# Kernel tuning notes

Hardware: AMD Instinct MI355X
Metric: run time of the kernel (lower is better)

The kernel has to match this reference:

```python
import jax, jax.numpy as jnp
import numpy as np
import math

V, D, H, DFF, NL, CTX = 32000, 512, 8, 2048, 2, 1024
B, S = 2, 1024

def ln(x, w, eps=1e-5):
    mu = jnp.mean(x, axis=-1, keepdims=True)
    var = jnp.var(x, axis=-1, keepdims=True)
    return (x - mu) / jnp.sqrt(var + eps) * w

def setup_inputs() -> dict:
    key = jax.random.key(0)
    ks = jax.random.split(key, 10)
    inp = {
        "x": jax.random.randint(ks[0], (B, S), 0, V),
        "wte": jax.random.normal(ks[1], (V, D), jnp.float32) * 0.02,
        "wpe": jax.random.normal(ks[2], (CTX + 1, D), jnp.float32) * 0.02,
        "ln_e_w": jnp.ones((D,), jnp.float32),
        "ln_p_w": jnp.ones((D,), jnp.float32),
        "ln_f_w": jnp.ones((D,), jnp.float32),
        "ln_mlp_w": jnp.ones((D,), jnp.float32),
        "W_q_diag": jax.random.normal(ks[3], (H, D), jnp.float32) * 0.02,
        "W_k_diag": jax.random.normal(ks[4], (H, D), jnp.float32) * 0.02,
        "W_o": jax.random.normal(ks[5], (NL, D, D * H), jnp.float32) * (0.02 / math.sqrt(2 * NL)),
        "mlp_w1": jax.random.normal(ks[6], (DFF, D), jnp.float32) * 0.02,
        "mlp_w2": jax.random.normal(ks[7], (D, DFF), jnp.float32) * 0.02,
    }
    return inp

def reference(x, wte, wpe, ln_e_w, ln_p_w, ln_f_w, ln_mlp_w, W_q_diag, W_k_diag, W_o, mlp_w1, mlp_w2):
    Bsz, Sl = x.shape
    e = ln(wte[x], ln_e_w)                       # (B,S,D)
    p = ln(wpe[: Sl + 1], ln_p_w)                # (S+1,D), identical across batch
    Q = p[1:][None, :, :] * W_q_diag[:, None, :]   # (H,S,D)
    K = p[:-1][None, :, :] * W_k_diag[:, None, :]  # (H,S,D)
    krn = jnp.einsum('hsd,htd->hst', Q, K) / math.sqrt(D)
    mask = jnp.tril(jnp.ones((Sl, Sl), bool))
    krn = jnp.where(mask[None], krn, 0.0)        # (H,S,S)
    wn = 1.0 / (jnp.arange(Sl, dtype=jnp.float32) + 1.0)  # W_N diagonal

    f_k = jnp.zeros_like(e)
    for i in range(NL):
        # R = softmax over S of (V,D)@(B,D,S) -> (B,V,S)
        R = jax.nn.softmax(jnp.einsum('vd,bsd->bvs', wte, f_k), axis=-1)
        ex_wte = jnp.einsum('bvs,vd->bsd', R, wte)
        ex_wte = ex_wte / jnp.sum(R, axis=1)[..., None]  # normalize by sum over V
        Vt = e - ex_wte                                   # (B,S,D)
        delta = jnp.einsum('hst,btd->bhsd', krn, Vt)      # (B,H,S,D)
        delta = delta * wn[None, None, :, None]           # W_N row scaling
        delta = jnp.transpose(delta, (0, 2, 1, 3)).reshape(Bsz, Sl, H * D)
        delta = delta @ W_o[i].T                          # (B,S,D)
        f_k = f_k + delta
        # use_ff MLP block
        h = ln(f_k, ln_mlp_w)
        f_k = f_k + jax.nn.gelu(h @ mlp_w1.T, approximate=False) @ mlp_w2.T

    out = ln(f_k, ln_f_w)
    logits = out[:, -1:, :] @ wte.T               # (B,1,V), targets=None branch
    return logits
```

## Files before the change

### kernel.cpp

```cpp
#include <hip/hip_runtime.h>

#define DV   512
#define SV   1024
#define BV   2
#define VV   32000
#define HV   8
#define DFFV 2048
#define NLV  2
#define KCX  25

typedef __bf16 bf16;
typedef __bf16 bf16x4 __attribute__((ext_vector_type(4)));
typedef __bf16 bf16x8 __attribute__((ext_vector_type(8)));
typedef float  f32x4  __attribute__((ext_vector_type(4)));

__device__ __forceinline__ void lds_dma16(const void* g, void* l) {
  __builtin_amdgcn_global_load_lds(
      (const __attribute__((address_space(1))) unsigned int*)g,
      (__attribute__((address_space(3))) unsigned int*)l,
      16, 0, 0);
}

template<typename OUT>
__device__ __forceinline__ void row_ln_512(const float* __restrict__ src,
                                           const float* __restrict__ w,
                                           OUT* __restrict__ dst, int lane) {
  const float4 a = *(const float4*)(src + lane*8);
  const float4 b = *(const float4*)(src + lane*8 + 4);
  float s = a.x+a.y+a.z+a.w + b.x+b.y+b.z+b.w;
  float q = a.x*a.x+a.y*a.y+a.z*a.z+a.w*a.w + b.x*b.x+b.y*b.y+b.z*b.z+b.w*b.w;
#pragma unroll
  for (int off = 32; off > 0; off >>= 1) {
    s += __shfl_down(s, off, 64);
    q += __shfl_down(q, off, 64);
  }
  s = __shfl(s, 0, 64); q = __shfl(q, 0, 64);
  const float mu   = s * (1.0f/512.0f);
  const float rstd = rsqrtf(q * (1.0f/512.0f) - mu*mu + 1e-5f);
  const float4 wa = *(const float4*)(w + lane*8);
  const float4 wb = *(const float4*)(w + lane*8 + 4);
  OUT* d = dst + lane*8;
  d[0] = (OUT)((a.x-mu)*rstd*wa.x);
  d[1] = (OUT)((a.y-mu)*rstd*wa.y);
  d[2] = (OUT)((a.z-mu)*rstd*wa.z);
  d[3] = (OUT)((a.w-mu)*rstd*wa.w);
  d[4] = (OUT)((b.x-mu)*rstd*wb.x);
  d[5] = (OUT)((b.y-mu)*rstd*wb.y);
  d[6] = (OUT)((b.z-mu)*rstd*wb.z);
  d[7] = (OUT)((b.w-mu)*rstd*wb.w);
}

__global__ void embed_ln_k(const int* __restrict__ x, const float* __restrict__ wte,
                           const float* __restrict__ w, float* __restrict__ e, int nrows) {
  int row = blockIdx.x * 4 + (threadIdx.x >> 6);
  if (row >= nrows) return;
  int tok = x[row];
  row_ln_512<float>(wte + (long)tok * DV, w, e + (long)row * DV, threadIdx.x & 63);
}

__global__ void rows_ln_f32_k(const float* __restrict__ src, const float* __restrict__ w,
                              float* __restrict__ dst, int nrows) {
  int row = blockIdx.x * 4 + (threadIdx.x >> 6);
  if (row >= nrows) return;
  row_ln_512<float>(src + (long)row * DV, w, dst + (long)row * DV, threadIdx.x & 63);
}

__global__ void rows_ln_bf16_k(const float* __restrict__ src, const float* __restrict__ w,
                               bf16* __restrict__ dst, int nrows) {
  int row = blockIdx.x * 4 + (threadIdx.x >> 6);
  if (row >= nrows) return;
  row_ln_512<bf16>(src + (long)row * DV, w, dst + (long)row * DV, threadIdx.x & 63);
}

__global__ void final_ln_k(const float* __restrict__ f_k, const float* __restrict__ w,
                           float* __restrict__ obuf) {
  int b = threadIdx.x >> 6;
  if (b >= BV) return;
  row_ln_512<float>(f_k + ((long)b * SV + (SV - 1)) * DV, w, obuf + (long)b * DV,
                    threadIdx.x & 63);
}

__global__ void cast_f2b_k(const float* __restrict__ in, bf16* __restrict__ o, long n) {
  long i = ((long)blockIdx.x * 256 + threadIdx.x) * 4;
  if (i >= n) return;
  float4 v = *(const float4*)(in + i);
  o[i+0] = (bf16)v.x; o[i+1] = (bf16)v.y; o[i+2] = (bf16)v.z; o[i+3] = (bf16)v.w;
}

__global__ void wte_prep_k(const float* __restrict__ wte, bf16* __restrict__ wb,
                           bf16* __restrict__ wbT, float* __restrict__ wm) {
  __shared__ float t[32][33];
  __shared__ float cpart[8][32];
  const int d0 = blockIdx.x * 32, v0 = blockIdx.y * 32;
  const int tx = threadIdx.x, ty = threadIdx.y;
  float csum = 0.f;
#pragma unroll
  for (int k = 0; k < 4; k++) {
    const int vl = ty*4 + k;
    const float val = wte[(long)(v0+vl)*DV + d0+tx];
    t[vl][tx] = val;
    csum += val;
  }
  cpart[ty][tx] = csum;
  __syncthreads();
  const int tid = ty*32 + tx;
  const int r = tid >> 3, c = (tid & 7) * 4;
  {
    bf16x4 o;
    o[0] = (bf16)t[r][c];   o[1] = (bf16)t[r][c+1];
    o[2] = (bf16)t[r][c+2]; o[3] = (bf16)t[r][c+3];
    *(bf16x4*)(&wb[(long)(v0+r)*DV + d0+c]) = o;
  }
  {
    bf16x4 o;
    o[0] = (bf16)t[c][r];   o[1] = (bf16)t[c+1][r];
    o[2] = (bf16)t[c+2][r]; o[3] = (bf16)t[c+3][r];
    *(bf16x4*)(&wbT[(long)(d0+r)*VV + v0+c]) = o;
  }
  if (ty == 0) {
    float s = 0.f;
#pragma unroll
    for (int k = 0; k < 8; k++) s += cpart[k][tx];
    atomicAdd(&wm[d0+tx], s);
  }
}

__global__ void qk_prep_k(const float* __restrict__ pn, const float* __restrict__ Wq,
                          const float* __restrict__ Wk, bf16* __restrict__ Qh,
                          bf16* __restrict__ Kh) {
  const int s = blockIdx.x, hh = blockIdx.y;
  const int d = threadIdx.x * 4;
  const float4 q  = *(const float4*)(pn + (long)(s+1)*DV + d);
  const float4 kk = *(const float4*)(pn + (long)s*DV + d);
  const float4 aq = *(const float4*)(Wq + (long)hh*DV + d);
  const float4 ak = *(const float4*)(Wk + (long)hh*DV + d);
  const long o = ((long)hh*SV + s)*DV + d;
  Qh[o+0]=(bf16)(q.x*aq.x);  Qh[o+1]=(bf16)(q.y*aq.y);
  Qh[o+2]=(bf16)(q.z*aq.z);  Qh[o+3]=(bf16)(q.w*aq.w);
  Kh[o+0]=(bf16)(kk.x*ak.x); Kh[o+1]=(bf16)(kk.y*ak.y);
  Kh[o+2]=(bf16)(kk.z*ak.z); Kh[o+3]=(bf16)(kk.w*ak.w);
}

__global__ void colsum_reduce_k(const float* __restrict__ part, float* __restrict__ cs) {
  const int s = blockIdx.x * 256 + threadIdx.x;
  float acc = 0.f;
  for (int v = 0; v < VV/128; v++) acc += part[(long)v * SV + s];
  cs[s] = acc;
}

__global__ void freduce_k(const float* __restrict__ part, float* __restrict__ f_k, int KC) {
  const long i = ((long)blockIdx.x * 256 + threadIdx.x) * 4;
  const int  b = (int)(i / ((long)SV*DV));
  const long r = i % ((long)SV*DV);
  float4 acc = *(const float4*)(f_k + i);
  for (int c = 0; c < KC; c++) {
    const float4 v = *(const float4*)(part + ((long)(b*KC + c))*SV*DV + r);
    acc.x += v.x; acc.y += v.y; acc.z += v.z; acc.w += v.w;
  }
  *(float4*)(f_k + i) = acc;
}

__global__ void vt_part_k(const float* __restrict__ e, const bf16* __restrict__ pb,
                          const float* __restrict__ cs, bf16* __restrict__ VtT) {
  __shared__ float t[32][33];
  const int d0 = blockIdx.x * 32, s0 = blockIdx.y * 32;
  const int tx = threadIdx.x, ty = threadIdx.y;
#pragma unroll
  for (int k = 0; k < 4; k++) {
    const int sl = ty + k*8;
    const long off = (long)(s0+sl)*DV + d0+tx;
    float acc = 0.f;
    for (int c = 0; c < KCX; c++) acc += (float)pb[(long)c*SV*DV + off];
    t[sl][tx] = e[off] - acc / cs[s0 + sl];
  }
  __syncthreads();
#pragma unroll
  for (int k = 0; k < 4; k++) {
    const int dl = ty + k*8;
    VtT[(long)(d0+dl)*SV + s0+tx] = (bf16)t[tx][dl];
  }
}

__global__ void vt0_transpose_k(const float* __restrict__ e, const float* __restrict__ wm,
                                bf16* __restrict__ VtT) {
  __shared__ float t[32][33];
  const int d0 = blockIdx.x * 32, s0 = blockIdx.y * 32;
  const int tx = threadIdx.x, ty = threadIdx.y;
  const float mval = wm[d0 + tx] * (1.0f / (float)VV);
#pragma unroll
  for (int k = 0; k < 4; k++) {
    const int sl = ty + k*8;
    t[sl][tx] = e[(long)(s0+sl)*DV + d0+tx] - mval;
  }
  __syncthreads();
#pragma unroll
  for (int k = 0; k < 4; k++) {
    const int dl = ty + k*8;
    VtT[(long)(d0+dl)*SV + s0+tx] = (bf16)t[tx][dl];
  }
}

__global__ void logits_k(const float* __restrict__ obuf, const float* __restrict__ wte,
                         float* __restrict__ out, int V) {
  const int wv = threadIdx.x >> 6, lane = threadIdx.x & 63;
  const int v = blockIdx.x * 4 + wv;
  const float* wr = wte + (long)v * DV;
  const float4 a  = *(const float4*)(wr + lane*8);
  const float4 c  = *(const float4*)(wr + lane*8 + 4);
  const float4 oa0 = *(const float4*)(obuf + lane*8);
  const float4 ob0 = *(const float4*)(obuf + lane*8 + 4);
  const float4 oa1 = *(const float4*)(obuf + DV + lane*8);
  const float4 ob1 = *(const float4*)(obuf + DV + lane*8 + 4);
  float d0 = a.x*oa0.x + a.y*oa0.y + a.z*oa0.z + a.w*oa0.w
           + c.x*ob0.x + c.y*ob0.y + c.z*ob0.z + c.w*ob0.w;
  float d1 = a.x*oa1.x + a.y*oa1.y + a.z*oa1.z + a.w*oa1.w
           + c.x*ob1.x + c.y*ob1.y + c.z*ob1.z + c.w*ob1.w;
#pragma unroll
  for (int off = 32; off > 0; off >>= 1) {
    d0 += __shfl_down(d0, off, 64);
    d1 += __shfl_down(d1, off, 64);
  }
  if (lane == 0) { out[v] = d0; out[(long)V + v] = d1; }
}

__device__ __forceinline__ long xcd_swz(long lin, long nwg) {
  const long qq = nwg >> 3, rr = nwg & 7;
  const long xcd = lin & 7, idx = lin >> 3;
  return (xcd < rr ? xcd * (qq + 1) : rr * (qq + 1) + (xcd - rr) * qq) + idx;
}

struct GemmArgs {
  const bf16* A; const bf16* B;
  float* Cf; bf16* Cb;
  int K, lda, ldb, ldc;
  long sAh, sAb, sBh, sBb, sCh, sCb;
  int Hmod, KC, causal, swap;
  float scale;
};

template<int EPI>
__global__ __launch_bounds__(256)
void gemm_nt(GemmArgs g) {
  __shared__ bf16 As[2][128*32];
  __shared__ bf16 Bs[2][128*32];
  const int tid = threadIdx.x;
  int bx = blockIdx.x, by = blockIdx.y, z = blockIdx.z;
  {
    const int nbx = gridDim.x, nby = gridDim.y;
    const long nwg = (long)nbx * nby * gridDim.z;
    long lin = xcd_swz(bx + (long)nbx * (by + (long)nby * z), nwg);
    bx = (int)(lin % nbx);
    const long t2 = lin / nbx;
    by = (int)(t2 % nby);
    z  = (int)(t2 / nby);
  }
  const int chunk = z % g.KC;
  const int zo = z / g.KC;
  const int h = zo % g.Hmod;
  const int b = zo / g.Hmod;
  if (g.swap) { int t = bx; bx = by; by = t; }
  const int m0 = by * 128;
  const int n0 = bx * 128;
  const long coff = (long)h * g.sCh + (long)b * g.sCb;

  if (EPI == 3 && n0 > m0 + 127) return;

  const bf16* A = g.A + (long)h * g.sAh + (long)b * g.sAb;
  const bf16* B = g.B + (long)h * g.sBh + (long)b * g.sBb;
  const int lane = tid & 63;
  const int wv = tid >> 6;
  const int wm = (wv >> 1) * 64;
  const int wn = (wv & 1) * 64;
  const int frow = lane & 15;
  const int quad = lane >> 4;
  const int sg8  = ((lane & 3) ^ ((lane >> 3) & 3)) * 8;
  const int drow = lane >> 2;

  const f32x4 fzero = {0.f, 0.f, 0.f, 0.f};
  f32x4 acc[4][4];
#pragma unroll
  for (int i = 0; i < 4; i++)
#pragma unroll
    for (int j = 0; j < 4; j++) acc[i][j] = fzero;

  int k0, klen;
  if (g.causal) { k0 = 0; klen = min(g.K, m0 + 128); }
  else          { klen = g.K / g.KC; k0 = chunk * klen; }

  auto stage = [&](int buf, int kk) {
#pragma unroll
    for (int c = 0; c < 2; c++) {
      const int rb = c*64 + wv*16;
      lds_dma16(A + (long)(m0 + rb + drow) * g.lda + kk + sg8, &As[buf][rb*32]);
      lds_dma16(B + (long)(n0 + rb + drow) * g.ldb + kk + sg8, &Bs[buf][rb*32]);
    }
  };

  const int nsteps = klen >> 5;
  int cur = 0;
  stage(0, k0);
  for (int it = 0; it < nsteps; ++it) {
    if (it + 1 < nsteps) {
      stage(cur ^ 1, k0 + (it + 1) * 32);
      asm volatile("s_waitcnt vmcnt(4)" ::: "memory");
    } else {
      asm volatile("s_waitcnt vmcnt(0)" ::: "memory");
    }
    __builtin_amdgcn_s_barrier();
    bf16x8 af[4], bfr[4];
    const int sw = (frow >> 1) & 3;
#pragma unroll
    for (int i = 0; i < 4; i++)
      af[i] = *(const bf16x8*)(&As[cur][(wm + i*16 + frow)*32 + ((quad ^ sw))*8]);
#pragma unroll
    for (int j = 0; j < 4; j++)
      bfr[j] = *(const bf16x8*)(&Bs[cur][(wn + j*16 + frow)*32 + ((quad ^ sw))*8]);
#pragma unroll
    for (int i = 0; i < 4; i++)
#pragma unroll
      for (int j = 0; j < 4; j++)
        acc[i][j] = __builtin_amdgcn_mfma_f32_16x16x32_bf16(af[i], bfr[j], acc[i][j], 0, 0, 0);
    __builtin_amdgcn_s_barrier();
    cur ^= 1;
  }

  const int rb = quad * 4;
#pragma unroll
  for (int i = 0; i < 4; i++) {
#pragma unroll
    for (int j = 0; j < 4; j++) {
#pragma unroll
      for (int r = 0; r < 4; r++) {
        const int gm = m0 + wm + i*16 + rb + r;
        const int gn = n0 + wn + j*16 + frow;
        const float v = acc[i][j][r];
        if (EPI == 2) {
          g.Cb[coff + (long)gm * g.ldc + gn] = (bf16)v;
        } else if (EPI == 3) {
          const float val = (gn <= gm) ? v * g.scale / (float)(gm + 1) : 0.0f;
          g.Cb[coff + (long)gm * g.ldc + gn] = (bf16)val;
        } else if (EPI == 4) {
          const float ge = 0.5f * v * (1.0f + erff(v * 0.70710678118f));
          g.Cb[coff + (long)gm * g.ldc + gn] = (bf16)ge;
        } else if (EPI == 6) {
          g.Cf[(long)(b*g.KC + chunk) * g.sCh + (long)gm * g.ldc + gn] = v;
        } else if (EPI == 7) {
          g.Cb[(long)chunk * g.sCh + (long)gm * g.ldc + gn] = (bf16)v;
        }
      }
    }
  }
}

template<int EPI>
__global__ __launch_bounds__(512)
void gemm256(GemmArgs g) {
  __shared__ bf16 As[2][256*64];
  __shared__ bf16 Bs[2][256*64];
  const int tid = threadIdx.x;
  int bm = blockIdx.x, bn = blockIdx.y, z = blockIdx.z;
  {
    const int nbx = gridDim.x, nby = gridDim.y;
    const long nwg = (long)nbx * nby * gridDim.z;
    long lin = xcd_swz(bm + (long)nbx * (bn + (long)nby * z), nwg);
    bm = (int)(lin % nbx);
    const long t2 = lin / nbx;
    bn = (int)(t2 % nby);
    z  = (int)(t2 / nby);
  }
  const int m0 = bm * 256, n0 = bn * 256;
  const int lane = tid & 63, wv = tid >> 6;
  const int wm = (wv >> 2) * 128, wn = (wv & 3) * 64;
  const int frow = lane & 15, quad = lane >> 4;
  const int sg8  = ((lane & 7) ^ (lane >> 3)) * 8;
  const int drow = lane >> 3;

  const f32x4 fzero = {0.f, 0.f, 0.f, 0.f};
  f32x4 acc[8][4];
#pragma unroll
  for (int i = 0; i < 8; i++)
#pragma unroll
    for (int j = 0; j < 4; j++) acc[i][j] = fzero;

  const int klen = g.K / g.KC;
  const int k0 = z * klen;

  auto stage = [&](int buf, int kk) {
#pragma unroll
    for (int c = 0; c < 4; c++) {
      const int rb = c*64 + wv*8;
      lds_dma16(g.A + (long)(m0 + rb + drow) * g.lda + kk + sg8, &As[buf][rb*64]);
      lds_dma16(g.B + (long)(n0 + rb + drow) * g.ldb + kk + sg8, &Bs[buf][rb*64]);
    }
  };

  const int nsteps = klen >> 6;
  int cur = 0;
  stage(0, k0);
  for (int it = 0; it < nsteps; ++it) {
    if (it + 1 < nsteps) {
      stage(cur ^ 1, k0 + (it + 1) * 64);
      asm volatile("s_waitcnt vmcnt(8)" ::: "memory");
    } else {
      asm volatile("s_waitcnt vmcnt(0)" ::: "memory");
    }
    __builtin_amdgcn_s_barrier();
    const int sw = frow & 7;
#pragma unroll
    for (int ks = 0; ks < 2; ks++) {
      bf16x8 af[8], bfr[4];
#pragma unroll
      for (int j = 0; j < 4; j++)
        bfr[j] = *(const bf16x8*)(&Bs[cur][(wn + j*16 + frow)*64 + (((ks*4 + quad) ^ sw))*8]);
#pragma unroll
      for (int i = 0; i < 8; i++)
        af[i] = *(const bf16x8*)(&As[cur][(wm + i*16 + frow)*64 + (((ks*4 + quad) ^ sw))*8]);
#pragma unroll
      for (int i = 0; i < 8; i++)
#pragma unroll
        for (int j = 0; j < 4; j++)
          acc[i][j] = __builtin_amdgcn_mfma_f32_16x16x32_bf16(af[i], bfr[j], acc[i][j], 0, 0, 0);
    }
    __builtin_amdgcn_s_barrier();
    cur ^= 1;
  }

  const int rb4 = quad * 4;
  if (EPI == 5) {
    const int vblk = (n0 + wn) >> 7;
#pragma unroll
    for (int i = 0; i < 8; i++) {
#pragma unroll
      for (int r = 0; r < 4; r++) {
        const int gm = m0 + wm + i*16 + rb4 + r;
        float rs = 0.f;
#pragma unroll
        for (int j = 0; j < 4; j++) {
          const int gn = n0 + wn + j*16 + frow;
          const float ev = __expf(acc[i][j][r]);
          g.Cb[(long)gm * g.ldc + gn] = (bf16)ev;
          rs += ev;
        }
#pragma unroll
        for (int off = 1; off < 16; off <<= 1)
          rs += __shfl_xor(rs, off, 64);
        if (frow == 0) atomicAdd(g.Cf + (long)vblk * SV + gm, rs);
      }
    }
  } else {
#pragma unroll
    for (int i = 0; i < 8; i++) {
#pragma unroll
      for (int j = 0; j < 4; j++) {
#pragma unroll
        for (int r = 0; r < 4; r++) {
          const int gm = m0 + wm + i*16 + rb4 + r;
          const int gn = n0 + wn + j*16 + frow;
          g.Cb[(long)z * g.sCh + (long)gm * g.ldc + gn] = (bf16)acc[i][j][r];
        }
      }
    }
  }
}

static void layer_tail(int il, bf16* krn, bf16* VtT, bf16* U_rs, bf16* Wo_b,
                       float* f_k, bf16* f_k_b, bf16* hbuf, bf16* Gbuf, float* fpart,
                       bf16* w1_b, bf16* w2_b, const float* lnmw, int do_cast,
                       hipStream_t stream) {
  {
    GemmArgs g = {};
    g.A = krn; g.B = VtT; g.Cb = U_rs;
    g.K = SV; g.lda = SV; g.ldb = SV; g.ldc = HV*DV;
    g.sAh = (long)SV*SV; g.sBb = (long)DV*SV;
    g.sCh = DV; g.sCb = (long)SV*HV*DV;
    g.Hmod = HV; g.KC = 1; g.causal = 1;
    gemm_nt<2><<<dim3(DV/128, SV/128, BV*HV), 256, 0, stream>>>(g);
  }
  {
    GemmArgs g = {};
    g.A = U_rs; g.B = Wo_b + (long)il*DV*HV*DV; g.Cf = fpart;
    g.K = HV*DV; g.lda = HV*DV; g.ldb = HV*DV; g.ldc = DV;
    g.sAb = (long)SV*HV*DV; g.sCh = (long)SV*DV;
    g.Hmod = 1; g.KC = 8; g.causal = 0;
    gemm_nt<6><<<dim3(DV/128, SV/128, BV*8), 256, 0, stream>>>(g);
  }
  freduce_k<<<dim3(BV*SV*DV/4/256), 256, 0, stream>>>(fpart, f_k, 8);
  rows_ln_bf16_k<<<dim3(BV*SV/4), 256, 0, stream>>>(f_k, lnmw, hbuf, BV*SV);
  {
    GemmArgs g = {};
    g.A = hbuf; g.B = w1_b; g.Cb = Gbuf;
    g.K = DV; g.lda = DV; g.ldb = DV; g.ldc = DFFV;
    g.sAb = (long)SV*DV; g.sCb = (long)SV*DFFV;
    g.Hmod = 1; g.KC = 1; g.causal = 0;
    gemm_nt<4><<<dim3(DFFV/128, SV/128, BV), 256, 0, stream>>>(g);
  }
  {
    GemmArgs g = {};
    g.A = Gbuf; g.B = w2_b; g.Cf = fpart;
    g.K = DFFV; g.lda = DFFV; g.ldb = DFFV; g.ldc = DV;
    g.sAb = (long)SV*DFFV; g.sCh = (long)SV*DV;
    g.Hmod = 1; g.KC = 8; g.causal = 0;
    gemm_nt<6><<<dim3(DV/128, SV/128, BV*8), 256, 0, stream>>>(g);
  }
  freduce_k<<<dim3(BV*SV*DV/4/256), 256, 0, stream>>>(fpart, f_k, 8);
  if (do_cast)
    cast_f2b_k<<<dim3((BV*SV*DV/4+255)/256), 256, 0, stream>>>(f_k, f_k_b, (long)BV*SV*DV);
}

extern "C" void kernel_launch(void* const* d_in, const int* in_sizes, int n_in,
                              void* d_out, int out_size, void* d_ws, size_t ws_size,
                              hipStream_t stream) {
  const int*   x    = (const int*)d_in[0];
  const float* wte  = (const float*)d_in[1];
  const float* wpe  = (const float*)d_in[2];
  const float* lnew = (const float*)d_in[3];
  const float* lnpw = (const float*)d_in[4];
  const float* lnfw = (const float*)d_in[5];
  const float* lnmw = (const float*)d_in[6];
  const float* Wq   = (const float*)d_in[7];
  const float* Wk   = (const float*)d_in[8];
  const float* Wo   = (const float*)d_in[9];
  const float* w1   = (const float*)d_in[10];
  const float* w2   = (const float*)d_in[11];
  float* out = (float*)d_out;
  (void)in_sizes; (void)n_in; (void)out_size; (void)ws_size;

  char* p = (char*)d_ws;
  auto alloc = [&](size_t bytes) -> void* {
    void* r = (void*)p;
    p += (bytes + 255) & ~(size_t)255;
    return r;
  };
  float* e      = (float*)alloc((size_t)BV*SV*DV*4);
  float* pn     = (float*)alloc((size_t)(SV+1)*DV*4);
  bf16*  wteT_b = (bf16*)alloc((size_t)DV*VV*2);
  bf16*  wte_b  = (bf16*)alloc((size_t)VV*DV*2);
  bf16*  krn    = (bf16*)alloc((size_t)HV*SV*SV*2);
  bf16*  Wo_b   = (bf16*)alloc((size_t)NLV*DV*HV*DV*2);
  bf16*  w1_b   = (bf16*)alloc((size_t)DFFV*DV*2);
  bf16*  w2_b   = (bf16*)alloc((size_t)DV*DFFV*2);
  float* f_k    = (float*)alloc((size_t)BV*SV*DV*4);
  bf16*  f_k_b  = (bf16*)alloc((size_t)BV*SV*DV*2);
  bf16*  expart = (bf16*)alloc((size_t)KCX*SV*DV*2);
  bf16*  VtT    = (bf16*)alloc((size_t)BV*DV*SV*2);
  bf16*  hbuf   = (bf16*)alloc((size_t)BV*SV*DV*2);
  float* colsum = (float*)alloc((size_t)SV*4);
  float* part   = (float*)alloc((size_t)(VV/128)*SV*4);
  float* obuf   = (float*)alloc((size_t)BV*DV*4);
  float* wmean  = (float*)alloc((size_t)DV*4);
  char*  arena  = (char*)alloc((size_t)SV*VV*2);
  bf16*  Qh     = (bf16*)arena;
  bf16*  Kh     = (bf16*)(arena + (size_t)HV*SV*DV*2);
  bf16*  PT     = (bf16*)arena;
  bf16*  U_rs   = (bf16*)arena;
  bf16*  Gbuf   = (bf16*)(arena + (size_t)BV*SV*HV*DV*2);
  float* fpart  = (float*)(arena + (size_t)BV*SV*HV*DV*2 + (size_t)BV*SV*DFFV*2);

  hipMemsetAsync(f_k,   0, (size_t)BV*SV*DV*4, stream);
  hipMemsetAsync(f_k_b, 0, (size_t)BV*SV*DV*2, stream);
  hipMemsetAsync(wmean, 0, (size_t)DV*4, stream);
  wte_prep_k<<<dim3(DV/32, VV/32), dim3(32,8), 0, stream>>>(wte, wte_b, wteT_b, wmean);
  cast_f2b_k<<<dim3((NLV*DV*HV*DV/4+255)/256), 256, 0, stream>>>(Wo, Wo_b, (long)NLV*DV*HV*DV);
  cast_f2b_k<<<dim3((DFFV*DV/4+255)/256), 256, 0, stream>>>(w1, w1_b, (long)DFFV*DV);
  cast_f2b_k<<<dim3((DV*DFFV/4+255)/256), 256, 0, stream>>>(w2, w2_b, (long)DV*DFFV);
  embed_ln_k<<<dim3(BV*SV/4), 256, 0, stream>>>(x, wte, lnew, e, BV*SV);
  rows_ln_f32_k<<<dim3((SV+1+3)/4), 256, 0, stream>>>(wpe, lnpw, pn, SV+1);
  qk_prep_k<<<dim3(SV, HV), 128, 0, stream>>>(pn, Wq, Wk, Qh, Kh);

  {
    GemmArgs g = {};
    g.A = Qh; g.B = Kh; g.Cb = krn;
    g.K = DV; g.lda = DV; g.ldb = DV; g.ldc = SV;
    g.sAh = (long)SV*DV; g.sBh = (long)SV*DV; g.sCh = (long)SV*SV;
    g.Hmod = HV; g.KC = 1; g.causal = 0;
    g.scale = 0.044194173824159216f;
    gemm_nt<3><<<dim3(SV/128, SV/128, HV), 256, 0, stream>>>(g);
  }

  for (int b = 0; b < BV; b++)
    vt0_transpose_k<<<dim3(DV/32, SV/32), dim3(32,8), 0, stream>>>(
        e + (long)b*SV*DV, wmean, VtT + (long)b*DV*SV);
  layer_tail(0, krn, VtT, U_rs, Wo_b, f_k, f_k_b, hbuf, Gbuf, fpart,
             w1_b, w2_b, lnmw, 1, stream);

  for (int b = 0; b < BV; b++) {
    hipMemsetAsync(part, 0, (size_t)(VV/128)*SV*4, stream);
    {
      GemmArgs g = {};
      g.A = f_k_b + (long)b*SV*DV; g.B = wte_b; g.Cb = PT; g.Cf = part;
      g.K = DV; g.lda = DV; g.ldb = DV; g.ldc = VV;
      g.KC = 1;
      gemm256<5><<<dim3(SV/256, VV/256, 1), 512, 0, stream>>>(g);
    }
    colsum_reduce_k<<<dim3(SV/256), 256, 0, stream>>>(part, colsum);
    {
      GemmArgs g = {};
      g.A = PT; g.B = wteT_b; g.Cb = expart;
      g.K = VV; g.lda = VV; g.ldb = VV; g.ldc = DV;
      g.sCh = (long)SV*DV;
      g.KC = KCX;
      gemm256<7><<<dim3(SV/256, DV/256, KCX), 512, 0, stream>>>(g);
    }
    vt_part_k<<<dim3(DV/32, SV/32), dim3(32,8), 0, stream>>>(
        e + (long)b*SV*DV, expart, colsum, VtT + (long)b*DV*SV);
  }
  layer_tail(1, krn, VtT, U_rs, Wo_b, f_k, f_k_b, hbuf, Gbuf, fpart,
             w1_b, w2_b, lnmw, 0, stream);

  final_ln_k<<<1, 256, 0, stream>>>(f_k, lnfw, obuf);
  logits_k<<<dim3(VV/4), 256, 0, stream>>>(obuf, wte, out, VV);
}
```

Baseline: 537.9 us.

## Restructure gemm256 main loop into 8-wave ping-pong with split-K LDS halves

Reorganizes the 256x256 GEMM kernel's LDS tiles into two 32-wide K halves per buffer and rewrites the main loop into four phases. Each phase interleaves finer-grained global->LDS DMA stages with LDS fragment loads and an MFMA cluster, using s_setprio and sched_barrier to separate memory and compute phases across waves. The swizzle pattern changes to fit the 32-element row layout. This aims to hide load latency and reduce register pressure by holding only four A fragments at a time, at the cost of more barriers per iteration and more fragile vmcnt bookkeeping.

```diff
diff --git a/kernel.cpp b/kernel.cpp
--- a/kernel.cpp
+++ b/kernel.cpp
@@ -355,8 +355,8 @@
 template<int EPI>
 __global__ __launch_bounds__(512)
 void gemm256(GemmArgs g) {
-  __shared__ bf16 As[2][256*64];
-  __shared__ bf16 Bs[2][256*64];
+  __shared__ bf16 As[2][2][256*32];
+  __shared__ bf16 Bs[2][2][256*32];
   const int tid = threadIdx.x;
   int bm = blockIdx.x, bn = blockIdx.y, z = blockIdx.z;
   {
@@ -372,8 +372,7 @@
   const int lane = tid & 63, wv = tid >> 6;
   const int wm = (wv >> 2) * 128, wn = (wv & 3) * 64;
   const int frow = lane & 15, quad = lane >> 4;
-  const int sg8  = ((lane & 7) ^ (lane >> 3)) * 8;
-  const int drow = lane >> 3;
+  const int sg8 = ((lane & 3) ^ ((lane >> 3) & 3)) * 8;
 
   const f32x4 fzero = {0.f, 0.f, 0.f, 0.f};
   f32x4 acc[8][4];
@@ -385,44 +384,103 @@
   const int klen = g.K / g.KC;
   const int k0 = z * klen;
 
-  auto stage = [&](int buf, int kk) {
-#pragma unroll
-    for (int c = 0; c < 4; c++) {
-      const int rb = c*64 + wv*8;
-      lds_dma16(g.A + (long)(m0 + rb + drow) * g.lda + kk + sg8, &As[buf][rb*64]);
-      lds_dma16(g.B + (long)(n0 + rb + drow) * g.ldb + kk + sg8, &Bs[buf][rb*64]);
+  auto stageA = [&](int slot, int ks, int kk) {
+#pragma unroll
+    for (int c = 0; c < 2; c++) {
+      const int rb = (wv*2 + c) * 16;
+      lds_dma16(g.A + (long)(m0 + rb + (lane >> 2)) * g.lda + kk + ks*32 + sg8,
+                &As[slot][ks][rb*32]);
     }
   };
+  auto stageB = [&](int slot, int ks, int kk) {
+#pragma unroll
+    for (int c = 0; c < 2; c++) {
+      const int rb = (wv*2 + c) * 16;
+      lds_dma16(g.B + (long)(n0 + rb + (lane >> 2)) * g.ldb + kk + ks*32 + sg8,
+                &Bs[slot][ks][rb*32]);
+    }
+  };
 
   const int nsteps = klen >> 6;
-  int cur = 0;
-  stage(0, k0);
+  const int sl = (quad ^ ((frow >> 1) & 3)) * 8;
+
+  stageA(0, 0, k0); stageB(0, 0, k0); stageA(0, 1, k0); stageB(0, 1, k0);
+
   for (int it = 0; it < nsteps; ++it) {
-    if (it + 1 < nsteps) {
-      stage(cur ^ 1, k0 + (it + 1) * 64);
-      asm volatile("s_waitcnt vmcnt(8)" ::: "memory");
-    } else {
-      asm volatile("s_waitcnt vmcnt(0)" ::: "memory");
-    }
-    __builtin_amdgcn_s_barrier();
-    const int sw = frow & 7;
-#pragma unroll
-    for (int ks = 0; ks < 2; ks++) {
-      bf16x8 af[8], bfr[4];
+    const int cur = it & 1, nxt = cur ^ 1;
+    const int kkn = k0 + (it + 1) * 64;
+    const bool pre = (it + 1 < nsteps);
+    bf16x8 bfr[4], af[4];
+    if (pre) { stageA(nxt, 0, kkn);
+               asm volatile("s_waitcnt vmcnt(6)" ::: "memory"); }
+    else     { asm volatile("s_waitcnt vmcnt(4)" ::: "memory"); }
+#pragma unroll
+    for (int j = 0; j < 4; j++)
+      bfr[j] = *(const bf16x8*)(&Bs[cur][0][(wn + j*16 + frow)*32 + sl]);
+#pragma unroll
+    for (int i = 0; i < 4; i++)
+      af[i] = *(const bf16x8*)(&As[cur][0][(wm + i*16 + frow)*32 + sl]);
+    __builtin_amdgcn_s_barrier();
+    asm volatile("s_waitcnt lgkmcnt(0)" ::: "memory");
+    __builtin_amdgcn_sched_barrier(0);
+    __builtin_amdgcn_s_setprio(1);
+#pragma unroll
+    for (int i = 0; i < 4; i++)
 #pragma unroll
       for (int j = 0; j < 4; j++)
-        bfr[j] = *(const bf16x8*)(&Bs[cur][(wn + j*16 + frow)*64 + (((ks*4 + quad) ^ sw))*8]);
-#pragma unroll
-      for (int i = 0; i < 8; i++)
-        af[i] = *(const bf16x8*)(&As[cur][(wm + i*16 + frow)*64 + (((ks*4 + quad) ^ sw))*8]);
-#pragma unroll
-      for (int i = 0; i < 8; i++)
-#pragma unroll
-        for (int j = 0; j < 4; j++)
-          acc[i][j] = __builtin_amdgcn_mfma_f32_16x16x32_bf16(af[i], bfr[j], acc[i][j], 0, 0, 0);
-    }
-    __builtin_amdgcn_s_barrier();
-    cur ^= 1;
+        acc[i][j] = __builtin_amdgcn_mfma_f32_16x16x32_bf16(af[i], bfr[j], acc[i][j], 0, 0, 0);
+    __builtin_amdgcn_s_setprio(0);
+    __builtin_amdgcn_s_barrier();
+    if (pre) stageB(nxt, 0, kkn);
+#pragma unroll
+    for (int i = 0; i < 4; i++)
+      af[i] = *(const bf16x8*)(&As[cur][0][(wm + (i+4)*16 + frow)*32 + sl]);
+    __builtin_amdgcn_s_barrier();
+    asm volatile("s_waitcnt lgkmcnt(0)" ::: "memory");
+    __builtin_amdgcn_sched_barrier(0);
+    __builtin_amdgcn_s_setprio(1);
+#pragma unroll
+    for (int i = 0; i < 4; i++)
+#pragma unroll
+      for (int j = 0; j < 4; j++)
+        acc[i+4][j] = __builtin_amdgcn_mfma_f32_16x16x32_bf16(af[i], bfr[j], acc[i+4][j], 0, 0, 0);
+    __builtin_amdgcn_s_setprio(0);
+    __builtin_amdgcn_s_barrier();
+    if (pre) { stageA(nxt, 1, kkn);
+               asm volatile("s_waitcnt vmcnt(6)" ::: "memory"); }
+    else     { asm volatile("s_waitcnt vmcnt(0)" ::: "memory"); }
+#pragma unroll
+    for (int j = 0; j < 4; j++)
+      bfr[j] = *(const bf16x8*)(&Bs[cur][1][(wn + j*16 + frow)*32 + sl]);
+#pragma unroll
+    for (int i = 0; i < 4; i++)
+      af[i] = *(const bf16x8*)(&As[cur][1][(wm + i*16 + frow)*32 + sl]);
+    __builtin_amdgcn_s_barrier();
+    asm volatile("s_waitcnt lgkmcnt(0)" ::: "memory");
+    __builtin_amdgcn_sched_barrier(0);
+    __builtin_amdgcn_s_setprio(1);
+#pragma unroll
+    for (int i = 0; i < 4; i++)
+#pragma unroll
+      for (int j = 0; j < 4; j++)
+        acc[i][j] = __builtin_amdgcn_mfma_f32_16x16x32_bf16(af[i], bfr[j], acc[i][j], 0, 0, 0);
+    __builtin_amdgcn_s_setprio(0);
+    __builtin_amdgcn_s_barrier();
+    if (pre) stageB(nxt, 1, kkn);
+#pragma unroll
+    for (int i = 0; i < 4; i++)
+      af[i] = *(const bf16x8*)(&As[cur][1][(wm + (i+4)*16 + frow)*32 + sl]);
+    __builtin_amdgcn_s_barrier();
+    asm volatile("s_waitcnt lgkmcnt(0)" ::: "memory");
+    __builtin_amdgcn_sched_barrier(0);
+    __builtin_amdgcn_s_setprio(1);
+#pragma unroll
+    for (int i = 0; i < 4; i++)
+#pragma unroll
+      for (int j = 0; j < 4; j++)
+        acc[i+4][j] = __builtin_amdgcn_mfma_f32_16x16x32_bf16(af[i], bfr[j], acc[i+4][j], 0, 0, 0);
+    __builtin_amdgcn_s_setprio(0);
+    __builtin_amdgcn_s_barrier();
   }
 
   const int rb4 = quad * 4;
```

Measured after the change: 569.3 us. 5.8% more time.

## Fuse reduce with layernorm/cast and stage gemm256 epilogue through LDS

Applied to the files above, without the earlier changes.

The split-K partial reduction now also applies the MLP layernorm and writes the bf16 input in the same pass, replacing separate freduce and rows_ln kernels. The second reduction casts f_k to bf16 inline instead of launching a separate cast kernel. The 256-tile GEMM epilogue writes results into swizzled shared memory and then stores 16-byte coalesced rows to global, instead of scattered 2-byte stores. This trades an extra barrier and LDS traffic for fewer launches and less global-memory traffic.

```diff
diff --git a/kernel.cpp b/kernel.cpp
--- a/kernel.cpp
+++ b/kernel.cpp
@@ -65,13 +65,6 @@
   row_ln_512<float>(src + (long)row * DV, w, dst + (long)row * DV, threadIdx.x & 63);
 }
 
-__global__ void rows_ln_bf16_k(const float* __restrict__ src, const float* __restrict__ w,
-                               bf16* __restrict__ dst, int nrows) {
-  int row = blockIdx.x * 4 + (threadIdx.x >> 6);
-  if (row >= nrows) return;
-  row_ln_512<bf16>(src + (long)row * DV, w, dst + (long)row * DV, threadIdx.x & 63);
-}
-
 __global__ void final_ln_k(const float* __restrict__ f_k, const float* __restrict__ w,
                            float* __restrict__ obuf) {
   int b = threadIdx.x >> 6;
@@ -148,7 +141,51 @@
   cs[s] = acc;
 }
 
-__global__ void freduce_k(const float* __restrict__ part, float* __restrict__ f_k, int KC) {
+__global__ void freduce_ln_k(const float* __restrict__ part, float* __restrict__ f_k,
+                             const float* __restrict__ w, bf16* __restrict__ hbuf, int KC) {
+  const int row = blockIdx.x * 4 + (threadIdx.x >> 6);
+  const int lane = threadIdx.x & 63;
+  const int b = row >> 10;
+  const long ro = (long)row * DV + lane*8;
+  const long po = (long)(row & (SV-1)) * DV + lane*8;
+  float v[8];
+  { const float4 a = *(const float4*)(f_k + ro);
+    const float4 c = *(const float4*)(f_k + ro + 4);
+    v[0]=a.x;v[1]=a.y;v[2]=a.z;v[3]=a.w;v[4]=c.x;v[5]=c.y;v[6]=c.z;v[7]=c.w; }
+  for (int c = 0; c < KC; c++) {
+    const float* pp = part + ((long)(b*KC + c))*SV*DV + po;
+    const float4 a = *(const float4*)pp;
+    const float4 d = *(const float4*)(pp + 4);
+    v[0]+=a.x;v[1]+=a.y;v[2]+=a.z;v[3]+=a.w;v[4]+=d.x;v[5]+=d.y;v[6]+=d.z;v[7]+=d.w;
+  }
+  { float4 o1={v[0],v[1],v[2],v[3]}, o2={v[4],v[5],v[6],v[7]};
+    *(float4*)(f_k + ro) = o1; *(float4*)(f_k + ro + 4) = o2; }
+  float s = 0.f, q = 0.f;
+#pragma unroll
+  for (int k = 0; k < 8; k++) { s += v[k]; q += v[k]*v[k]; }
+#pragma unroll
+  for (int off = 32; off > 0; off >>= 1) {
+    s += __shfl_down(s, off, 64);
+    q += __shfl_down(q, off, 64);
+  }
+  s = __shfl(s, 0, 64); q = __shfl(q, 0, 64);
+  const float mu   = s * (1.0f/512.0f);
+  const float rstd = rsqrtf(q * (1.0f/512.0f) - mu*mu + 1e-5f);
+  const float4 wa = *(const float4*)(w + lane*8);
+  const float4 wb = *(const float4*)(w + lane*8 + 4);
+  bf16* d = hbuf + (long)row * DV + lane*8;
+  d[0] = (bf16)((v[0]-mu)*rstd*wa.x);
+  d[1] = (bf16)((v[1]-mu)*rstd*wa.y);
+  d[2] = (bf16)((v[2]-mu)*rstd*wa.z);
+  d[3] = (bf16)((v[3]-mu)*rstd*wa.w);
+  d[4] = (bf16)((v[4]-mu)*rstd*wb.x);
+  d[5] = (bf16)((v[5]-mu)*rstd*wb.y);
+  d[6] = (bf16)((v[6]-mu)*rstd*wb.z);
+  d[7] = (bf16)((v[7]-mu)*rstd*wb.w);
+}
+
+__global__ void freduce_cast_k(const float* __restrict__ part, float* __restrict__ f_k,
+                               bf16* __restrict__ fb, int KC, int do_cast) {
   const long i = ((long)blockIdx.x * 256 + threadIdx.x) * 4;
   const int  b = (int)(i / ((long)SV*DV));
   const long r = i % ((long)SV*DV);
@@ -158,6 +195,10 @@
     acc.x += v.x; acc.y += v.y; acc.z += v.z; acc.w += v.w;
   }
   *(float4*)(f_k + i) = acc;
+  if (do_cast) {
+    bf16x4 o; o[0]=(bf16)acc.x; o[1]=(bf16)acc.y; o[2]=(bf16)acc.z; o[3]=(bf16)acc.w;
+    *(bf16x4*)(&fb[i]) = o;
+  }
 }
 
 __global__ void vt_part_k(const float* __restrict__ e, const bf16* __restrict__ pb,
@@ -344,8 +385,6 @@
           g.Cb[coff + (long)gm * g.ldc + gn] = (bf16)ge;
         } else if (EPI == 6) {
           g.Cf[(long)(b*g.KC + chunk) * g.sCh + (long)gm * g.ldc + gn] = v;
-        } else if (EPI == 7) {
-          g.Cb[(long)chunk * g.sCh + (long)gm * g.ldc + gn] = (bf16)v;
         }
       }
     }
@@ -355,8 +394,7 @@
 template<int EPI>
 __global__ __launch_bounds__(512)
 void gemm256(GemmArgs g) {
-  __shared__ bf16 As[2][256*64];
-  __shared__ bf16 Bs[2][256*64];
+  __shared__ bf16 sh[2][2][256*64];
   const int tid = threadIdx.x;
   int bm = blockIdx.x, bn = blockIdx.y, z = blockIdx.z;
   {
@@ -389,8 +427,8 @@
 #pragma unroll
     for (int c = 0; c < 4; c++) {
       const int rb = c*64 + wv*8;
-      lds_dma16(g.A + (long)(m0 + rb + drow) * g.lda + kk + sg8, &As[buf][rb*64]);
-      lds_dma16(g.B + (long)(n0 + rb + drow) * g.ldb + kk + sg8, &Bs[buf][rb*64]);
+      lds_dma16(g.A + (long)(m0 + rb + drow) * g.lda + kk + sg8, &sh[0][buf][rb*64]);
+      lds_dma16(g.B + (long)(n0 + rb + drow) * g.ldb + kk + sg8, &sh[1][buf][rb*64]);
     }
   };
 
@@ -411,10 +449,10 @@
       bf16x8 af[8], bfr[4];
 #pragma unroll
       for (int j = 0; j < 4; j++)
-        bfr[j] = *(const bf16x8*)(&Bs[cur][(wn + j*16 + frow)*64 + (((ks*4 + quad) ^ sw))*8]);
+        bfr[j] = *(const bf16x8*)(&sh[1][cur][(wn + j*16 + frow)*64 + (((ks*4 + quad) ^ sw))*8]);
 #pragma unroll
       for (int i = 0; i < 8; i++)
-        af[i] = *(const bf16x8*)(&As[cur][(wm + i*16 + frow)*64 + (((ks*4 + quad) ^ sw))*8]);
+        af[i] = *(const bf16x8*)(&sh[0][cur][(wm + i*16 + frow)*64 + (((ks*4 + quad) ^ sw))*8]);
 #pragma unroll
       for (int i = 0; i < 8; i++)
 #pragma unroll
@@ -425,41 +463,38 @@
     cur ^= 1;
   }
 
+  bf16* epi = &sh[0][0][0];
   const int rb4 = quad * 4;
-  if (EPI == 5) {
-    const int vblk = (n0 + wn) >> 7;
-#pragma unroll
-    for (int i = 0; i < 8; i++) {
-#pragma unroll
-      for (int r = 0; r < 4; r++) {
-        const int gm = m0 + wm + i*16 + rb4 + r;
-        float rs = 0.f;
-#pragma unroll
-        for (int j = 0; j < 4; j++) {
-          const int gn = n0 + wn + j*16 + frow;
-          const float ev = __expf(acc[i][j][r]);
-          g.Cb[(long)gm * g.ldc + gn] = (bf16)ev;
-          rs += ev;
-        }
+  const int vblk = (n0 + wn) >> 7;
+#pragma unroll
+  for (int i = 0; i < 8; i++) {
+#pragma unroll
+    for (int r = 0; r < 4; r++) {
+      const int row = wm + i*16 + rb4 + r;
+      float rs = 0.f;
+#pragma unroll
+      for (int j = 0; j < 4; j++) {
+        const int col = wn + j*16 + frow;
+        float v = acc[i][j][r];
+        if (EPI == 5) { v = __expf(v); rs += v; }
+        epi[row*256 + (((col >> 3) ^ (row & 7)) << 3) + (col & 7)] = (bf16)v;
+      }
+      if (EPI == 5) {
 #pragma unroll
         for (int off = 1; off < 16; off <<= 1)
           rs += __shfl_xor(rs, off, 64);
-        if (frow == 0) atomicAdd(g.Cf + (long)vblk * SV + gm, rs);
+        if (frow == 0) atomicAdd(g.Cf + (long)vblk * SV + (m0 + row), rs);
       }
     }
-  } else {
-#pragma unroll
-    for (int i = 0; i < 8; i++) {
-#pragma unroll
-      for (int j = 0; j < 4; j++) {
-#pragma unroll
-        for (int r = 0; r < 4; r++) {
-          const int gm = m0 + wm + i*16 + rb4 + r;
-          const int gn = n0 + wn + j*16 + frow;
-          g.Cb[(long)z * g.sCh + (long)gm * g.ldc + gn] = (bf16)acc[i][j][r];
-        }
-      }
-    }
+  }
+  __syncthreads();
+  bf16* dst = (EPI == 5) ? g.Cb : (g.Cb + (long)z * g.sCh);
+#pragma unroll
+  for (int k = 0; k < 16; k++) {
+    const int row = wv*32 + k*2 + (lane >> 5);
+    const int chk = lane & 31;
+    const bf16x8 vv = *(const bf16x8*)(&epi[row*256 + ((chk ^ (row & 7)) << 3)]);
+    *(bf16x8*)(&dst[(long)(m0 + row) * g.ldc + n0 + chk*8]) = vv;
   }
 }
 
@@ -484,8 +519,7 @@
     g.Hmod = 1; g.KC = 8; g.causal = 0;
     gemm_nt<6><<<dim3(DV/128, SV/128, BV*8), 256, 0, stream>>>(g);
   }
-  freduce_k<<<dim3(BV*SV*DV/4/256), 256, 0, stream>>>(fpart, f_k, 8);
-  rows_ln_bf16_k<<<dim3(BV*SV/4), 256, 0, stream>>>(f_k, lnmw, hbuf, BV*SV);
+  freduce_ln_k<<<dim3(BV*SV/4), 256, 0, stream>>>(fpart, f_k, lnmw, hbuf, 8);
   {
     GemmArgs g = {};
     g.A = hbuf; g.B = w1_b; g.Cb = Gbuf;
@@ -502,9 +536,7 @@
     g.Hmod = 1; g.KC = 8; g.causal = 0;
     gemm_nt<6><<<dim3(DV/128, SV/128, BV*8), 256, 0, stream>>>(g);
   }
-  freduce_k<<<dim3(BV*SV*DV/4/256), 256, 0, stream>>>(fpart, f_k, 8);
-  if (do_cast)
-    cast_f2b_k<<<dim3((BV*SV*DV/4+255)/256), 256, 0, stream>>>(f_k, f_k_b, (long)BV*SV*DV);
+  freduce_cast_k<<<dim3(BV*SV*DV/4/256), 256, 0, stream>>>(fpart, f_k, f_k_b, 8, do_cast);
 }
 
 extern "C" void kernel_launch(void* const* d_in, const int* in_sizes, int n_in,
```

After: 527.0 us. -2.0%, faster.
